# Kernel tuning notes

Measured on AMD Instinct MI355X. Metric: run time of the kernel, lower is better.

## Reference

```python
import jax, jax.numpy as jnp
import numpy as np

OUT_FEATURES = 11008
IN_FEATURES = 4096
GROUP_SIZE = 128
NUM_GROUPS = OUT_FEATURES * IN_FEATURES // GROUP_SIZE  # 352256

NF4_VALUES = jnp.array([
    -1.0, -0.6961928009986877, -0.5250730514526367, -0.39491748809814453,
    -0.28444138169288635, -0.18477343022823334, -0.09105003625154495, 0.0,
    0.07958029955625534, 0.16093020141124725, 0.24611230194568634,
    0.33791524171829224, 0.44070982933044434, 0.5626170039176941,
    0.7229568362236023, 1.0], dtype=jnp.float32)


def setup_inputs() -> dict:
    key = jax.random.key(0)
    k1, k2, k3, k4 = jax.random.split(key, 4)
    x = jax.random.normal(k1, (4, 2048, IN_FEATURES), dtype=jnp.float32)
    weight_quant = jax.random.randint(k2, (OUT_FEATURES * IN_FEATURES,), 0, 16, dtype=jnp.int32)
    weight_scale = jax.random.uniform(k3, (NUM_GROUPS,), dtype=jnp.float32) * 0.05 + 1e-3
    bias = jax.random.normal(k4, (OUT_FEATURES,), dtype=jnp.float32)
    return {"x": x, "weight_quant": weight_quant, "weight_scale": weight_scale, "bias": bias}


def reference(x, weight_quant, weight_scale, bias):
    # NF4 dequantization: table lookup, then per-group (of 128 consecutive flat
    # elements) scale multiply, then reshape to [out_features, in_features].
    idx = jnp.clip(weight_quant, 0, 15)
    w = NF4_VALUES.astype(x.dtype)[idx]                      # flat [OUT*IN]
    w = (w.reshape(NUM_GROUPS, GROUP_SIZE)
         * weight_scale.astype(x.dtype)[:, None])
    w = w.reshape(OUT_FEATURES, IN_FEATURES)
    # F.linear: x @ W^T + b
    out = jnp.einsum('bsi,oi->bso', x, w) + bias.astype(x.dtype)
    return out
```

## Files before the change

### kernel.cpp

```cpp
#include <hip/hip_runtime.h>
#include <hip/hip_bf16.h>
#include <stdint.h>
#include <stddef.h>

#define OUT_F  11008
#define IN_F   4096
#define M_ROWS 8192

typedef __bf16 bf16;
typedef __attribute__((ext_vector_type(8))) __bf16 bf16x8;
typedef __attribute__((ext_vector_type(4))) float floatx4;

__device__ const float NF4_TAB[16] = {
    -1.0f, -0.6961928009986877f, -0.5250730514526367f, -0.39491748809814453f,
    -0.28444138169288635f, -0.18477343022823334f, -0.09105003625154495f, 0.0f,
    0.07958029955625534f, 0.16093020141124725f, 0.24611230194568634f,
    0.33791524171829224f, 0.44070982933044434f, 0.5626170039176941f,
    0.7229568362236023f, 1.0f};

__global__ __launch_bounds__(256) void cvt_x_kernel(const float* __restrict__ x,
                                                    bf16* __restrict__ xb) {
    size_t t = (size_t)blockIdx.x * 256 + threadIdx.x;
    const float4* xv = (const float4*)x;
    float4 a = xv[2 * t];
    float4 b = xv[2 * t + 1];
    bf16x8 o;
    o[0] = (bf16)a.x; o[1] = (bf16)a.y; o[2] = (bf16)a.z; o[3] = (bf16)a.w;
    o[4] = (bf16)b.x; o[5] = (bf16)b.y; o[6] = (bf16)b.z; o[7] = (bf16)b.w;
    *(bf16x8*)(xb + 8 * t) = o;
}

__global__ __launch_bounds__(256) void dequant_kernel(const int* __restrict__ q,
                                                      const float* __restrict__ sc,
                                                      bf16* __restrict__ wb) {
    __shared__ float tab[16];
    if (threadIdx.x < 16) tab[threadIdx.x] = NF4_TAB[threadIdx.x];
    __syncthreads();
    size_t t = (size_t)blockIdx.x * 256 + threadIdx.x;
    const int4* qv = (const int4*)q;
    int4 a = qv[2 * t];
    int4 b = qv[2 * t + 1];
    float s = sc[t >> 4];
    bf16x8 o;
    o[0] = (bf16)(tab[a.x & 15] * s); o[1] = (bf16)(tab[a.y & 15] * s);
    o[2] = (bf16)(tab[a.z & 15] * s); o[3] = (bf16)(tab[a.w & 15] * s);
    o[4] = (bf16)(tab[b.x & 15] * s); o[5] = (bf16)(tab[b.y & 15] * s);
    o[6] = (bf16)(tab[b.z & 15] * s); o[7] = (bf16)(tab[b.w & 15] * s);
    *(bf16x8*)(wb + 8 * t) = o;
}

#define BM 256
#define BN 256
#define BK 32
#define NT (IN_F / BK)
#define GRID ((M_ROWS / BM) * (OUT_F / BN))

static __device__ __forceinline__ void gload_lds16(const void* g, void* l) {
    __builtin_amdgcn_global_load_lds((const __attribute__((address_space(1))) void*)g,
                                     (__attribute__((address_space(3))) void*)l,
                                     16, 0, 0);
}

__global__ __launch_bounds__(512, 2) void gemm_bias_kernel(const bf16* __restrict__ A,
                                                           const bf16* __restrict__ B,
                                                           const float* __restrict__ bias,
                                                           float* __restrict__ C) {
    __shared__ bf16 sA[4][BM * BK];
    __shared__ bf16 sB[4][BN * BK];

    const int tid  = threadIdx.x;
    const int w    = tid >> 6;
    const int lane = tid & 63;
    const int wm   = w >> 2;
    const int wn   = w & 3;
    const int l16  = lane & 15;
    const int quad = lane >> 4;

    const int bid = blockIdx.x;
    const int swz = (bid & 7) * (GRID / 8) + (bid >> 3);
    const int tm  = swz / (OUT_F / BN);
    const int tn  = swz % (OUT_F / BN);
    const int bm  = tm * BM;
    const int bn  = tn * BN;

    const int lr = lane >> 2;
    const int ls = (lane & 3) ^ (lr & 3);
    const bf16* aG = A + (size_t)(bm + w * 32 + lr) * IN_F + ls * 8;
    const bf16* bG = B + (size_t)(bn + w * 32 + lr) * IN_F + ls * 8;

    const int soff = (quad ^ (l16 & 3)) * 8;
    const int aOff = (wm * 128 + l16) * BK + soff;
    const int bOff = (wn * 64 + l16) * BK + soff;

    floatx4 acc[8][4] = {};

    auto stage = [&](int tt) {
        bf16* la = &sA[tt & 3][w * 1024];
        bf16* lb = &sB[tt & 3][w * 1024];
        const bf16* ga = aG + (size_t)tt * BK;
        const bf16* gb = bG + (size_t)tt * BK;
        gload_lds16(ga, la);
        gload_lds16(ga + (size_t)16 * IN_F, la + 512);
        gload_lds16(gb, lb);
        gload_lds16(gb + (size_t)16 * IN_F, lb + 512);
    };

    auto compute = [&](int t) {
        const bf16* bufA = sA[t & 3];
        const bf16* bufB = sB[t & 3];
        bf16x8 bfrg[4], afrg[4];
#pragma unroll
        for (int nt = 0; nt < 4; ++nt)
            bfrg[nt] = *(const bf16x8*)(bufB + bOff + nt * 512);
#pragma unroll
        for (int mt = 0; mt < 4; ++mt)
            afrg[mt] = *(const bf16x8*)(bufA + aOff + mt * 512);
        asm volatile("s_waitcnt lgkmcnt(0)" ::: "memory");
        __builtin_amdgcn_s_setprio(1);
#pragma unroll
        for (int mt = 0; mt < 4; ++mt)
#pragma unroll
            for (int nt = 0; nt < 4; ++nt)
                acc[mt][nt] = __builtin_amdgcn_mfma_f32_16x16x32_bf16(
                    afrg[mt], bfrg[nt], acc[mt][nt], 0, 0, 0);
        __builtin_amdgcn_s_setprio(0);
#pragma unroll
        for (int mt = 0; mt < 4; ++mt)
            afrg[mt] = *(const bf16x8*)(bufA + aOff + (mt + 4) * 512);
        asm volatile("s_waitcnt lgkmcnt(0)" ::: "memory");
        __builtin_amdgcn_s_setprio(1);
#pragma unroll
        for (int mt = 0; mt < 4; ++mt)
#pragma unroll
            for (int nt = 0; nt < 4; ++nt)
                acc[mt + 4][nt] = __builtin_amdgcn_mfma_f32_16x16x32_bf16(
                    afrg[mt], bfrg[nt], acc[mt + 4][nt], 0, 0, 0);
        __builtin_amdgcn_s_setprio(0);
    };

    stage(0); stage(1); stage(2);

    for (int t = 0; t < NT - 3; ++t) {
        asm volatile("s_waitcnt vmcnt(8)" ::: "memory");
        __builtin_amdgcn_s_barrier();
        stage(t + 3);
        compute(t);
    }
    asm volatile("s_waitcnt vmcnt(8)" ::: "memory");
    __builtin_amdgcn_s_barrier();
    compute(NT - 3);
    asm volatile("s_waitcnt vmcnt(4)" ::: "memory");
    __builtin_amdgcn_s_barrier();
    compute(NT - 2);
    asm volatile("s_waitcnt vmcnt(0)" ::: "memory");
    __builtin_amdgcn_s_barrier();
    compute(NT - 1);

#pragma unroll
    for (int nt = 0; nt < 4; ++nt) {
        int col = bn + wn * 64 + nt * 16 + l16;
        float bv = bias[col];
#pragma unroll
        for (int mt = 0; mt < 8; ++mt) {
            int row0 = bm + wm * 128 + mt * 16 + quad * 4;
#pragma unroll
            for (int r = 0; r < 4; ++r)
                C[(size_t)(row0 + r) * OUT_F + col] = acc[mt][nt][r] + bv;
        }
    }
}

#define FBM 64
#define FBN 64
#define FBK 64
__global__ __launch_bounds__(256) void fallback_gemm(const float* __restrict__ x,
                                                     const int* __restrict__ q,
                                                     const float* __restrict__ sc,
                                                     const float* __restrict__ bias,
                                                     float* __restrict__ out) {
    __shared__ float sA[FBM][FBK + 1];
    __shared__ float sB[FBN][FBK + 1];
    const int tx = threadIdx.x & 15, ty = threadIdx.x >> 4;
    const int bm = blockIdx.y * FBM, bn = blockIdx.x * FBN;
    float acc[4][4] = {};
    for (int k0 = 0; k0 < IN_F; k0 += FBK) {
        for (int i = threadIdx.x; i < FBM * (FBK / 4); i += 256) {
            int r = i / (FBK / 4), c4 = (i % (FBK / 4)) * 4;
            float4 v = *(const float4*)&x[(size_t)(bm + r) * IN_F + k0 + c4];
            sA[r][c4] = v.x; sA[r][c4 + 1] = v.y; sA[r][c4 + 2] = v.z; sA[r][c4 + 3] = v.w;
            size_t fi = (size_t)(bn + r) * IN_F + k0 + c4;
            int4 qv = *(const int4*)&q[fi];
            float s = sc[fi >> 7];
            sB[r][c4]     = NF4_TAB[qv.x & 15] * s;
            sB[r][c4 + 1] = NF4_TAB[qv.y & 15] * s;
            sB[r][c4 + 2] = NF4_TAB[qv.z & 15] * s;
            sB[r][c4 + 3] = NF4_TAB[qv.w & 15] * s;
        }
        __syncthreads();
        for (int k = 0; k < FBK; ++k) {
            float av[4], bvv[4];
#pragma unroll
            for (int i = 0; i < 4; ++i) av[i] = sA[ty * 4 + i][k];
#pragma unroll
            for (int j = 0; j < 4; ++j) bvv[j] = sB[tx * 4 + j][k];
#pragma unroll
            for (int i = 0; i < 4; ++i)
#pragma unroll
                for (int j = 0; j < 4; ++j) acc[i][j] += av[i] * bvv[j];
        }
        __syncthreads();
    }
#pragma unroll
    for (int i = 0; i < 4; ++i)
#pragma unroll
        for (int j = 0; j < 4; ++j)
            out[(size_t)(bm + ty * 4 + i) * OUT_F + bn + tx * 4 + j] =
                acc[i][j] + bias[bn + tx * 4 + j];
}

extern "C" void kernel_launch(void* const* d_in, const int* in_sizes, int n_in,
                              void* d_out, int out_size, void* d_ws, size_t ws_size,
                              hipStream_t stream) {
    const float* x    = (const float*)d_in[0];
    const int*   q    = (const int*)d_in[1];
    const float* sc   = (const float*)d_in[2];
    const float* bias = (const float*)d_in[3];
    float* out = (float*)d_out;

    const size_t xb_bytes = (size_t)M_ROWS * IN_F * sizeof(bf16);
    const size_t wb_bytes = (size_t)OUT_F * IN_F * sizeof(bf16);

    if (ws_size >= xb_bytes + wb_bytes) {
        bf16* xb = (bf16*)d_ws;
        bf16* wb = (bf16*)((char*)d_ws + xb_bytes);
        cvt_x_kernel<<<(M_ROWS * IN_F) / (8 * 256), 256, 0, stream>>>(x, xb);
        dequant_kernel<<<(OUT_F * IN_F) / (8 * 256), 256, 0, stream>>>(q, sc, wb);
        gemm_bias_kernel<<<GRID, 512, 0, stream>>>(xb, wb, bias, out);
    } else {
        fallback_gemm<<<dim3(OUT_F / FBN, M_ROWS / FBM), 256, 0, stream>>>(x, q, sc, bias, out);
    }
}
```

Before: 1.539 ms.

## Restructure GEMM mainloop to BK=64 double-buffered quadrant schedule with fragment reuse

Doubles the K tile to 64 and replaces the 4-stage BK=32 ring with a 2-stage double buffer split into A/B halves. Each iteration runs four quadrant phases, reusing A and B register fragments across phases and issuing the next tile's global-to-LDS loads between phases. It also changes the LDS layout and XOR swizzle. The aim is fewer barriers per K and better overlap of loads with MFMA. In exchange it adds more barriers within each iteration and a shallower prefetch depth.

```diff
diff --git a/kernel.cpp b/kernel.cpp
--- a/kernel.cpp
+++ b/kernel.cpp
@@ -51,7 +51,7 @@
 
 #define BM 256
 #define BN 256
-#define BK 32
+#define BK 64
 #define NT (IN_F / BK)
 #define GRID ((M_ROWS / BM) * (OUT_F / BN))
 
@@ -65,8 +65,8 @@
                                                            const bf16* __restrict__ B,
                                                            const float* __restrict__ bias,
                                                            float* __restrict__ C) {
-    __shared__ bf16 sA[4][BM * BK];
-    __shared__ bf16 sB[4][BN * BK];
+    __shared__ bf16 sA[2][2][8192];
+    __shared__ bf16 sB[2][2][8192];
 
     const int tid  = threadIdx.x;
     const int w    = tid >> 6;
@@ -83,78 +83,94 @@
     const int bm  = tm * BM;
     const int bn  = tn * BN;
 
-    const int lr = lane >> 2;
-    const int ls = (lane & 3) ^ (lr & 3);
-    const bf16* aG = A + (size_t)(bm + w * 32 + lr) * IN_F + ls * 8;
-    const bf16* bG = B + (size_t)(bn + w * 32 + lr) * IN_F + ls * 8;
-
-    const int soff = (quad ^ (l16 & 3)) * 8;
-    const int aOff = (wm * 128 + l16) * BK + soff;
-    const int bOff = (wn * 64 + l16) * BK + soff;
+    const int p0   = w * 2048 + lane * 16;
+    const int l0   = p0 ^ (((p0 >> 9) & 1) << 5);
+    const int srow = l0 >> 7;
+    const int scol = (l0 & 127) >> 1;
+    const bf16* aSrc = A + (size_t)(bm + srow) * IN_F + scol;
+    const bf16* bSrc = B + (size_t)(bn + srow) * IN_F + scol;
+
+    auto stage = [&](int ts, int hf) {
+        const int c    = ts & 1;
+        const int half = hf >> 1;
+        const bf16* src = (hf & 1) ? bSrc : aSrc;
+        bf16* dst = (hf & 1) ? &sB[c][half][0] : &sA[c][half][0];
+        const bf16* s0 = src + (size_t)(half * 128) * IN_F + (size_t)ts * BK;
+        gload_lds16(s0, dst + w * 1024);
+        gload_lds16(s0 + (size_t)8 * IN_F, dst + w * 1024 + 512);
+    };
+
+    const int xr = ((l16 >> 2) & 1) << 5;
+    const int tA = (l16 * 128 + quad * 16) ^ xr;
+    const int tB = ((wn & 1) * 8192 + l16 * 128 + quad * 16) ^ xr;
 
     floatx4 acc[8][4] = {};
-
-    auto stage = [&](int tt) {
-        bf16* la = &sA[tt & 3][w * 1024];
-        bf16* lb = &sB[tt & 3][w * 1024];
-        const bf16* ga = aG + (size_t)tt * BK;
-        const bf16* gb = bG + (size_t)tt * BK;
-        gload_lds16(ga, la);
-        gload_lds16(ga + (size_t)16 * IN_F, la + 512);
-        gload_lds16(gb, lb);
-        gload_lds16(gb + (size_t)16 * IN_F, lb + 512);
-    };
-
-    auto compute = [&](int t) {
-        const bf16* bufA = sA[t & 3];
-        const bf16* bufB = sB[t & 3];
-        bf16x8 bfrg[4], afrg[4];
-#pragma unroll
-        for (int nt = 0; nt < 4; ++nt)
-            bfrg[nt] = *(const bf16x8*)(bufB + bOff + nt * 512);
-#pragma unroll
-        for (int mt = 0; mt < 4; ++mt)
-            afrg[mt] = *(const bf16x8*)(bufA + aOff + mt * 512);
-        asm volatile("s_waitcnt lgkmcnt(0)" ::: "memory");
-        __builtin_amdgcn_s_setprio(1);
-#pragma unroll
-        for (int mt = 0; mt < 4; ++mt)
-#pragma unroll
-            for (int nt = 0; nt < 4; ++nt)
-                acc[mt][nt] = __builtin_amdgcn_mfma_f32_16x16x32_bf16(
-                    afrg[mt], bfrg[nt], acc[mt][nt], 0, 0, 0);
-        __builtin_amdgcn_s_setprio(0);
-#pragma unroll
-        for (int mt = 0; mt < 4; ++mt)
-            afrg[mt] = *(const bf16x8*)(bufA + aOff + (mt + 4) * 512);
-        asm volatile("s_waitcnt lgkmcnt(0)" ::: "memory");
-        __builtin_amdgcn_s_setprio(1);
-#pragma unroll
-        for (int mt = 0; mt < 4; ++mt)
-#pragma unroll
-            for (int nt = 0; nt < 4; ++nt)
-                acc[mt + 4][nt] = __builtin_amdgcn_mfma_f32_16x16x32_bf16(
-                    afrg[mt], bfrg[nt], acc[mt + 4][nt], 0, 0, 0);
-        __builtin_amdgcn_s_setprio(0);
-    };
-
-    stage(0); stage(1); stage(2);
-
-    for (int t = 0; t < NT - 3; ++t) {
-        asm volatile("s_waitcnt vmcnt(8)" ::: "memory");
-        __builtin_amdgcn_s_barrier();
-        stage(t + 3);
-        compute(t);
-    }
-    asm volatile("s_waitcnt vmcnt(8)" ::: "memory");
-    __builtin_amdgcn_s_barrier();
-    compute(NT - 3);
-    asm volatile("s_waitcnt vmcnt(4)" ::: "memory");
-    __builtin_amdgcn_s_barrier();
-    compute(NT - 2);
+    bf16x8 af[4][2];
+    bf16x8 b01[2][2];
+    bf16x8 b23[2][2];
+
+#define RD_A(c, f, ks) (*(const bf16x8*)((const char*)&sA[c][wm][0] + tA + (f) * 2048 + (ks) * 64))
+#define RD_B(c, f, ks) (*(const bf16x8*)((const char*)&sB[c][wn >> 1][0] + tB + (f) * 2048 + (ks) * 64))
+
+#define QUADRANT(MB, BV, NB)                                                     \
+    do {                                                                         \
+        _Pragma("unroll") for (int ks = 0; ks < 2; ++ks)                         \
+        _Pragma("unroll") for (int mf = 0; mf < 4; ++mf)                         \
+        _Pragma("unroll") for (int nf = 0; nf < 2; ++nf)                         \
+            acc[(MB) + mf][(NB) + nf] = __builtin_amdgcn_mfma_f32_16x16x32_bf16( \
+                af[mf][ks], BV[nf][ks], acc[(MB) + mf][(NB) + nf], 0, 0, 0);     \
+    } while (0)
+
+#define PHASE_SYNC()                                  \
+    __builtin_amdgcn_s_barrier();                     \
+    asm volatile("s_waitcnt lgkmcnt(0)");             \
+    __builtin_amdgcn_sched_barrier(0)
+
+    stage(0, 0); stage(0, 1); stage(0, 2); stage(0, 3);
     asm volatile("s_waitcnt vmcnt(0)" ::: "memory");
     __builtin_amdgcn_s_barrier();
-    compute(NT - 1);
+
+    for (int T = 0; T < NT; ++T) {
+        const int cur = T & 1;
+        const bool pf = (T + 1 < NT);
+
+#pragma unroll
+        for (int f = 0; f < 4; ++f) { af[f][0] = RD_A(cur, f, 0); af[f][1] = RD_A(cur, f, 1); }
+#pragma unroll
+        for (int f = 0; f < 2; ++f) { b01[f][0] = RD_B(cur, f, 0); b01[f][1] = RD_B(cur, f, 1); }
+        if (pf) { stage(T + 1, 0); stage(T + 1, 1); }
+        PHASE_SYNC();
+        __builtin_amdgcn_s_setprio(1);
+        QUADRANT(0, b01, 0);
+        __builtin_amdgcn_s_setprio(0);
+        __builtin_amdgcn_s_barrier();
+
+#pragma unroll
+        for (int f = 0; f < 2; ++f) { b23[f][0] = RD_B(cur, f + 2, 0); b23[f][1] = RD_B(cur, f + 2, 1); }
+        if (pf) { stage(T + 1, 2); stage(T + 1, 3); }
+        PHASE_SYNC();
+        __builtin_amdgcn_s_setprio(1);
+        QUADRANT(0, b23, 2);
+        __builtin_amdgcn_s_setprio(0);
+        __builtin_amdgcn_s_barrier();
+
+#pragma unroll
+        for (int f = 0; f < 4; ++f) { af[f][0] = RD_A(cur, f + 4, 0); af[f][1] = RD_A(cur, f + 4, 1); }
+        PHASE_SYNC();
+        __builtin_amdgcn_s_setprio(1);
+        QUADRANT(4, b23, 2);
+        __builtin_amdgcn_s_setprio(0);
+        __builtin_amdgcn_s_barrier();
+
+#pragma unroll
+        for (int f = 0; f < 2; ++f) { b01[f][0] = RD_B(cur, f, 0); b01[f][1] = RD_B(cur, f, 1); }
+        PHASE_SYNC();
+        __builtin_amdgcn_s_setprio(1);
+        QUADRANT(4, b01, 0);
+        __builtin_amdgcn_s_setprio(0);
+        if (pf) asm volatile("s_waitcnt vmcnt(0)" ::: "memory");
+        __builtin_amdgcn_s_barrier();
+    }
 
 #pragma unroll
     for (int nt = 0; nt < 4; ++nt) {
@@ -168,6 +184,10 @@
                 C[(size_t)(row0 + r) * OUT_F + col] = acc[mt][nt][r] + bv;
         }
     }
+#undef RD_A
+#undef RD_B
+#undef QUADRANT
+#undef PHASE_SYNC
 }
 
 #define FBM 64
```

New measurement: 1.427 ms. 7.3% less time.
